# Kernel optimization log

Hardware: AMD Instinct MI355X
Metric: run time of the kernel (lower is better)

## Reference

```python
import jax, jax.numpy as jnp
import numpy as np

N_ITERS = 3  # Set2Set n_iters


def _set2set(feat, gid, B, Wih, Whh, bih, bhh):
    # DGL Set2Set with n_iters=3, n_layers=1: LSTM(input=2D, hidden=D), PyTorch gate order i,f,g,o
    N, D = feat.shape
    q_star = jnp.zeros((B, 2 * D), feat.dtype)
    h = jnp.zeros((B, D), feat.dtype)
    c = jnp.zeros((B, D), feat.dtype)
    bias = bih + bhh
    for _ in range(N_ITERS):
        gates = q_star @ Wih.T + h @ Whh.T + bias  # (B, 4D)
        i, f, g, o = jnp.split(gates, 4, axis=-1)
        i = jax.nn.sigmoid(i); f = jax.nn.sigmoid(f); o = jax.nn.sigmoid(o); g = jnp.tanh(g)
        c = f * c + i * g
        h = o * jnp.tanh(c)  # q = h, shape (B, D)
        e = jnp.sum(feat * h[gid], axis=-1)  # (N,) attention logits
        m = jax.ops.segment_max(e, gid, num_segments=B, indices_are_sorted=True)
        ex = jnp.exp(e - m[gid])
        s = jax.ops.segment_sum(ex, gid, num_segments=B, indices_are_sorted=True)
        alpha = ex / s[gid]  # segment softmax
        readout = jax.ops.segment_sum(feat * alpha[:, None], gid, num_segments=B, indices_are_sorted=True)
        q_star = jnp.concatenate([h, readout], axis=-1)  # (B, 2D)
    return q_star


def setup_inputs() -> dict:
    key = jax.random.key(0)
    ks = jax.random.split(key, 18)
    N, E, D, B, OUT = 100000, 1000000, 64, 64, 1
    s = 1.0 / np.sqrt(D)
    u = lambda k, shp, b: jax.random.uniform(k, shp, jnp.float32, -b, b)
    inp = {
        'feat': jax.random.normal(ks[0], (N, D), jnp.float32),
        'efeat': jax.random.normal(ks[1], (E, D), jnp.float32),
        'edge_dst': jax.random.randint(ks[2], (E,), 0, N, jnp.int32),
        'node_graph': jnp.sort(jax.random.randint(ks[3], (N,), 0, B, jnp.int32)),
        'n_graphs': B,
        'node_Wih': u(ks[4], (4 * D, 2 * D), s), 'node_Whh': u(ks[5], (4 * D, D), s),
        'node_bih': u(ks[6], (4 * D,), s), 'node_bhh': u(ks[7], (4 * D,), s),
        'edge_Wih': u(ks[8], (4 * D, 2 * D), s), 'edge_Whh': u(ks[9], (4 * D, D), s),
        'edge_bih': u(ks[10], (4 * D,), s), 'edge_bhh': u(ks[11], (4 * D,), s),
        'W1': u(ks[12], (32, 4 * D), np.sqrt(6.0 / (4 * D + 32)) * np.sqrt(2.0)),
        'b1': jnp.zeros((32,), jnp.float32),
        'W2': u(ks[13], (16, 32), np.sqrt(6.0 / 48) * np.sqrt(2.0)),
        'b2': jnp.zeros((16,), jnp.float32),
        'W3': u(ks[14], (OUT, 16), np.sqrt(6.0 / (16 + OUT)) * np.sqrt(2.0)),
        'b3': jnp.zeros((OUT,), jnp.float32),
    }
    return inp


def reference(feat, efeat, edge_dst, node_graph, n_graphs,
              node_Wih, node_Whh, node_bih, node_bhh,
              edge_Wih, edge_Whh, edge_bih, edge_bhh,
              W1, b1, W2, b2, W3, b3):
    N = feat.shape[0]
    # mpnn = identity: node_emb = feat, edge_emb = efeat
    node_s2s = _set2set(feat, node_graph, n_graphs, node_Wih, node_Whh, node_bih, node_bhh)
    # graph.update_all(fn.copy_e, fn.mean): scatter-mean of edge features onto dst nodes
    deg = jax.ops.segment_sum(jnp.ones((efeat.shape[0],), feat.dtype), edge_dst, num_segments=N)
    edge_agg = jax.ops.segment_sum(efeat, edge_dst, num_segments=N) / jnp.maximum(deg, 1.0)[:, None]
    edge_s2s = _set2set(edge_agg, node_graph, n_graphs, edge_Wih, edge_Whh, edge_bih, edge_bhh)
    out = jnp.concatenate([node_s2s, edge_s2s], axis=1)  # (B, 4D)
    out = jax.nn.relu(out @ W1.T + b1)
    out = jax.nn.relu(out @ W2.T + b2)
    out = out @ W3.T + b3
    return out
```

## Files before the change

kernel.cpp:

```cpp
#include <hip/hip_runtime.h>
#include <math.h>

#define D 64
#define B 64
#define NPB 256
#define NSLOT 4
#define SCAN_BS 1024

__device__ __forceinline__ unsigned encf(float x) {
  unsigned u = __float_as_uint(x);
  return (u & 0x80000000u) ? ~u : (u | 0x80000000u);
}
__device__ __forceinline__ float decf(unsigned e) {
  return (e & 0x80000000u) ? __uint_as_float(e ^ 0x80000000u) : __uint_as_float(~e);
}
__device__ __forceinline__ float sigm(float x) { return 1.0f / (1.0f + expf(-x)); }


__global__ void k_deg(const int* __restrict__ edge_dst, int* __restrict__ deg, int E) {
  int i = blockIdx.x * blockDim.x + threadIdx.x;
  if (i < E) atomicAdd(&deg[edge_dst[i]], 1);
}

__global__ void k_scan1(const int* __restrict__ deg, int* __restrict__ row_start,
                        int* __restrict__ blocksum, int N) {
  __shared__ int sm[SCAN_BS];
  int t = threadIdx.x;
  int base = blockIdx.x * SCAN_BS;
  int v = (base + t < N) ? deg[base + t] : 0;
  sm[t] = v;
  __syncthreads();
  for (int ofs = 1; ofs < SCAN_BS; ofs <<= 1) {
    int add = (t >= ofs) ? sm[t - ofs] : 0;
    __syncthreads();
    sm[t] += add;
    __syncthreads();
  }
  if (base + t < N) row_start[base + t] = sm[t] - v;
  if (t == SCAN_BS - 1) blocksum[blockIdx.x] = sm[t];
}

__global__ void k_scan2(int* __restrict__ blocksum, int nb) {
  __shared__ int sm[128];
  int t = threadIdx.x;
  int v = (t < nb) ? blocksum[t] : 0;
  sm[t] = v;
  __syncthreads();
  for (int ofs = 1; ofs < 128; ofs <<= 1) {
    int add = (t >= ofs) ? sm[t - ofs] : 0;
    __syncthreads();
    sm[t] += add;
    __syncthreads();
  }
  if (t < nb) blocksum[t] = sm[t] - v;
}

__global__ void k_scan3(int* __restrict__ row_start, const int* __restrict__ blocksum,
                        int* __restrict__ cursor, int N) {
  int n = blockIdx.x * blockDim.x + threadIdx.x;
  if (n < N) {
    int v = row_start[n] + blocksum[n / SCAN_BS];
    row_start[n] = v;
    cursor[n] = v;
  }
}

__global__ void k_fill(const int* __restrict__ edge_dst, int* __restrict__ cursor,
                       int* __restrict__ csr, int E) {
  int e = blockIdx.x * blockDim.x + threadIdx.x;
  if (e < E) {
    int dst = edge_dst[e];
    int idx = atomicAdd(&cursor[dst], 1);
    csr[idx] = e;
  }
}


struct AttSmem {
  float r_lds[16 * NSLOT * D];
  float s_lds[16 * NSLOT];
  float m_lds[16 * NSLOT];
  float h_lds[NSLOT * D];
  float o_lds[NSLOT];
  int used[NSLOT];
  int sg_first;
};

__device__ __forceinline__ void att_body(AttSmem* sm, const float* __restrict__ F,
                                         const int* __restrict__ gid,
                                         const float* __restrict__ h,
                                         const float* __restrict__ off,
                                         unsigned* __restrict__ m_enc,
                                         float* __restrict__ s_buf,
                                         float* __restrict__ r_buf,
                                         int N, int bx) {
  const int tid = threadIdx.x;
  const int grp = tid >> 4;
  const int d4  = tid & 15;
  const int base = bx * NPB;

  for (int i = tid; i < 16 * NSLOT * D; i += 256) sm->r_lds[i] = 0.0f;
  if (tid < 16 * NSLOT) { sm->s_lds[tid] = 0.0f; sm->m_lds[tid] = -3.4e38f; }
  if (tid < NSLOT) sm->used[tid] = 0;
  if (tid == 0) sm->sg_first = gid[base];
  __syncthreads();
  const int gfirst = sm->sg_first;
  {
    int slot = tid >> 6, dim = tid & 63;
    int g = gfirst + slot;
    if (g < B) {
      sm->h_lds[tid] = h[g * D + dim];
      if (dim == 0) sm->o_lds[slot] = off[g];
    }
  }
  __syncthreads();

  float4 acc = make_float4(0.f, 0.f, 0.f, 0.f);
  float sum_ex = 0.0f;
  float local_max = -3.4e38f;
  int cur_g = -1;

  for (int itn = 0; itn < NPB / 32; ++itn) {
    int n0 = base + itn * 32 + grp;
    int n1 = n0 + 16;
    bool ok0 = n0 < N, ok1 = n1 < N;
    int g0 = ok0 ? gid[n0] : -1;
    int g1 = ok1 ? gid[n1] : -1;
    float4 f0 = make_float4(0,0,0,0), f1 = make_float4(0,0,0,0);
    float dot0 = 0.f, dot1 = 0.f, ex0 = 0.f, ex1 = 0.f;
    if (ok0) {
      f0 = *(const float4*)(F + (size_t)n0 * D + d4 * 4);
      int s0 = g0 - gfirst;
      float4 hv = (s0 >= 0 && s0 < NSLOT) ? *(const float4*)&sm->h_lds[(s0 << 6) + (d4 << 2)]
                                          : *(const float4*)(h + (size_t)g0 * D + d4 * 4);
      dot0 = f0.x * hv.x + f0.y * hv.y + f0.z * hv.z + f0.w * hv.w;
    }
    if (ok1) {
      f1 = *(const float4*)(F + (size_t)n1 * D + d4 * 4);
      int s1 = g1 - gfirst;
      float4 hv = (s1 >= 0 && s1 < NSLOT) ? *(const float4*)&sm->h_lds[(s1 << 6) + (d4 << 2)]
                                          : *(const float4*)(h + (size_t)g1 * D + d4 * 4);
      dot1 = f1.x * hv.x + f1.y * hv.y + f1.z * hv.z + f1.w * hv.w;
    }
    dot0 += __shfl_xor(dot0, 1); dot1 += __shfl_xor(dot1, 1);
    dot0 += __shfl_xor(dot0, 2); dot1 += __shfl_xor(dot1, 2);
    dot0 += __shfl_xor(dot0, 4); dot1 += __shfl_xor(dot1, 4);
    dot0 += __shfl_xor(dot0, 8); dot1 += __shfl_xor(dot1, 8);
    if (ok0) {
      int s0 = g0 - gfirst;
      ex0 = expf(dot0 - ((s0 >= 0 && s0 < NSLOT) ? sm->o_lds[s0] : off[g0]));
    }
    if (ok1) {
      int s1 = g1 - gfirst;
      ex1 = expf(dot1 - ((s1 >= 0 && s1 < NSLOT) ? sm->o_lds[s1] : off[g1]));
    }

    #pragma unroll
    for (int pair = 0; pair < 2; ++pair) {
      bool ok = pair ? ok1 : ok0;
      int g = pair ? g1 : g0;
      float ex = pair ? ex1 : ex0;
      float dt = pair ? dot1 : dot0;
      float4 f = pair ? f1 : f0;
      if (!ok) continue;
      if (g != cur_g) {
        if (cur_g >= 0) {
          int slot = cur_g - gfirst;
          if (slot >= 0 && slot < NSLOT) {
            float4* p = (float4*)&sm->r_lds[((grp * NSLOT + slot) << 6) + (d4 << 2)];
            float4 v = *p;
            v.x += acc.x; v.y += acc.y; v.z += acc.z; v.w += acc.w;
            *p = v;
            if (d4 == 0) {
              sm->s_lds[grp * NSLOT + slot] += sum_ex;
              sm->m_lds[grp * NSLOT + slot] = fmaxf(sm->m_lds[grp * NSLOT + slot], local_max);
              sm->used[slot] = 1;
            }
          } else {
            float* rp = r_buf + cur_g * D + d4 * 4;
            atomicAdd(rp + 0, acc.x); atomicAdd(rp + 1, acc.y);
            atomicAdd(rp + 2, acc.z); atomicAdd(rp + 3, acc.w);
            if (d4 == 0) { atomicAdd(&s_buf[cur_g], sum_ex); atomicMax(&m_enc[cur_g], encf(local_max)); }
          }
        }
        cur_g = g; acc = make_float4(0,0,0,0); sum_ex = 0.f; local_max = -3.4e38f;
      }
      acc.x += ex * f.x; acc.y += ex * f.y; acc.z += ex * f.z; acc.w += ex * f.w;
      if (d4 == 0) { sum_ex += ex; local_max = fmaxf(local_max, dt); }
    }
  }
  if (cur_g >= 0) {
    int slot = cur_g - gfirst;
    if (slot >= 0 && slot < NSLOT) {
      float4* p = (float4*)&sm->r_lds[((grp * NSLOT + slot) << 6) + (d4 << 2)];
      float4 v = *p;
      v.x += acc.x; v.y += acc.y; v.z += acc.z; v.w += acc.w;
      *p = v;
      if (d4 == 0) {
        sm->s_lds[grp * NSLOT + slot] += sum_ex;
        sm->m_lds[grp * NSLOT + slot] = fmaxf(sm->m_lds[grp * NSLOT + slot], local_max);
        sm->used[slot] = 1;
      }
    } else {
      float* rp = r_buf + cur_g * D + d4 * 4;
      atomicAdd(rp + 0, acc.x); atomicAdd(rp + 1, acc.y);
      atomicAdd(rp + 2, acc.z); atomicAdd(rp + 3, acc.w);
      if (d4 == 0) { atomicAdd(&s_buf[cur_g], sum_ex); atomicMax(&m_enc[cur_g], encf(local_max)); }
    }
  }
  __syncthreads();

  {
    int slot = tid >> 6, dim = tid & 63;
    int g = gfirst + slot;
    if (g < B && sm->used[slot]) {
      float sum = 0.0f;
      #pragma unroll
      for (int q = 0; q < 16; ++q) sum += sm->r_lds[((q * NSLOT + slot) << 6) + dim];
      atomicAdd(&r_buf[g * D + dim], sum);
    }
  }
  if (tid < NSLOT) {
    int g = gfirst + tid;
    if (g < B && sm->used[tid]) {
      float ssum = 0.0f;
      #pragma unroll
      for (int q = 0; q < 16; ++q) ssum += sm->s_lds[q * NSLOT + tid];
      atomicAdd(&s_buf[g], ssum);
    }
  } else if (tid >= 64 && tid < 64 + NSLOT) {
    int slot = tid - 64;
    int g = gfirst + slot;
    if (g < B && sm->used[slot]) {
      float mmax = -3.4e38f;
      #pragma unroll
      for (int q = 0; q < 16; ++q) mmax = fmaxf(mmax, sm->m_lds[q * NSLOT + slot]);
      atomicMax(&m_enc[g], encf(mmax));
    }
  }
}

__device__ __forceinline__ void gather_body(const float* __restrict__ efeat,
                                            const int* __restrict__ csr,
                                            const int* __restrict__ row_start,
                                            const int* __restrict__ deg,
                                            float* __restrict__ edge_agg, int N, int bx) {
  int grp = (bx * 256 + threadIdx.x) >> 4;
  int l16 = threadIdx.x & 15;
  if (grp >= N) return;
  int base = row_start[grp];
  int dg = deg[grp];
  float4 acc = make_float4(0.f, 0.f, 0.f, 0.f);
  for (int i = 0; i < dg; i += 16) {
    int idx[16];
    #pragma unroll
    for (int j = 0; j < 16; ++j) {
      int k = i + j;
      idx[j] = csr[base + (k < dg ? k : dg - 1)];
    }
    #pragma unroll
    for (int j = 0; j < 16; ++j) {
      float4 v = *(const float4*)(efeat + (size_t)idx[j] * D + l16 * 4);
      bool ok = (i + j < dg);
      acc.x += ok ? v.x : 0.0f;
      acc.y += ok ? v.y : 0.0f;
      acc.z += ok ? v.z : 0.0f;
      acc.w += ok ? v.w : 0.0f;
    }
  }
  float inv = 1.0f / fmaxf((float)dg, 1.0f);
  acc.x *= inv; acc.y *= inv; acc.z *= inv; acc.w *= inv;
  *(float4*)(edge_agg + (size_t)grp * D + l16 * 4) = acc;
}

__global__ void k_gather_att0(int GB, const float* __restrict__ efeat,
                              const int* __restrict__ csr, const int* __restrict__ row_start,
                              const int* __restrict__ deg, float* __restrict__ edge_agg,
                              const float* __restrict__ feat, const int* __restrict__ gid,
                              const float* __restrict__ h2, const float* __restrict__ off2,
                              unsigned* __restrict__ m2, float* __restrict__ s2,
                              float* __restrict__ r2, int N) {
  __shared__ AttSmem sm;
  if ((int)blockIdx.x < GB) {
    gather_body(efeat, csr, row_start, deg, edge_agg, N, blockIdx.x);
  } else {
    att_body(&sm, feat, gid, h2, off2, m2, s2, r2, N, blockIdx.x - GB);
  }
}

__global__ void k_att(int side_base, const float* __restrict__ feat,
                      const float* __restrict__ edge_agg, const int* __restrict__ gid,
                      const float* __restrict__ h2, const float* __restrict__ off2,
                      unsigned* __restrict__ m2, float* __restrict__ s2,
                      float* __restrict__ r2, int N) {
  __shared__ AttSmem sm;
  int side = blockIdx.y + side_base;
  att_body(&sm, side ? edge_agg : feat, gid, h2 + side * B * D, off2 + side * B,
           m2 + side * B, s2 + side * B, r2 + side * B * D, N, blockIdx.x);
}


__global__ void k_lstm(int firstN, int firstE, int side_base,
                       float* __restrict__ h2, float* __restrict__ c2,
                       float* __restrict__ s2, float* __restrict__ r2,
                       unsigned* __restrict__ m2, float* __restrict__ off2,
                       const float* __restrict__ nWih, const float* __restrict__ nWhh,
                       const float* __restrict__ nbih, const float* __restrict__ nbhh,
                       const float* __restrict__ eWih, const float* __restrict__ eWhh,
                       const float* __restrict__ ebih, const float* __restrict__ ebhh) {
  __shared__ float lq[2 * D], lsg[4 * D];
  int side = blockIdx.y + side_base;
  int first = side ? firstE : firstN;
  const float* Wih = side ? eWih : nWih;
  const float* Whh = side ? eWhh : nWhh;
  const float* bih = side ? ebih : nbih;
  const float* bhh = side ? ebhh : nbhh;
  float* h = h2 + side * B * D;
  float* c = c2 + side * B * D;
  float* s_buf = s2 + side * B;
  float* r_buf = r2 + side * B * D;
  unsigned* m_enc = m2 + side * B;
  float* off = off2 + side * B;

  int b = blockIdx.x, j = threadIdx.x;
  if (j < D) {
    lq[j] = h[b * D + j];
  } else if (j < 2 * D) {
    lq[j] = first ? 0.0f : (r_buf[b * D + (j - D)] / s_buf[b]);
  }
  __syncthreads();
  float acc = bih[j] + bhh[j];
  const float* wr = Wih + (size_t)j * (2 * D);
  #pragma unroll 8
  for (int k = 0; k < 2 * D; ++k) acc += lq[k] * wr[k];
  const float* wr2 = Whh + (size_t)j * D;
  #pragma unroll 8
  for (int k = 0; k < D; ++k) acc += lq[k] * wr2[k];
  lsg[j] = acc;
  __syncthreads();
  if (j < D) {
    float ig = sigm(lsg[j]);
    float fg = sigm(lsg[D + j]);
    float gg = tanhf(lsg[2 * D + j]);
    float og = sigm(lsg[3 * D + j]);
    float cn = fg * c[b * D + j] + ig * gg;
    c[b * D + j] = cn;
    h[b * D + j] = og * tanhf(cn);
    r_buf[b * D + j] = 0.0f;
  }
  if (j == D) s_buf[b] = 0.0f;
  if (j == D + 1) {
    off[b] = first ? 0.0f : decf(m_enc[b]);
    m_enc[b] = 0u;
  }
}


__global__ void k_mlp(const float* __restrict__ h2, const float* __restrict__ r2,
                      const float* __restrict__ s2,
                      const float* __restrict__ W1, const float* __restrict__ b1,
                      const float* __restrict__ W2, const float* __restrict__ b2,
                      const float* __restrict__ W3, const float* __restrict__ b3,
                      float* __restrict__ out) {
  __shared__ float x[4 * D], h1[32], h2s[16];
  int b = blockIdx.x, t = threadIdx.x;
  x[t]       = (t < D) ? h2[b * D + t]         : r2[b * D + (t - D)] / s2[b];
  x[128 + t] = (t < D) ? h2[B * D + b * D + t] : r2[B * D + b * D + (t - D)] / s2[B + b];
  __syncthreads();
  if (t < 32) {
    float acc = b1[t];
    const float* w = W1 + (size_t)t * (4 * D);
    #pragma unroll 8
    for (int k = 0; k < 4 * D; ++k) acc += x[k] * w[k];
    h1[t] = fmaxf(acc, 0.0f);
  }
  __syncthreads();
  if (t < 16) {
    float acc = b2[t];
    const float* w = W2 + (size_t)t * 32;
    #pragma unroll
    for (int k = 0; k < 32; ++k) acc += h1[k] * w[k];
    h2s[t] = fmaxf(acc, 0.0f);
  }
  __syncthreads();
  if (t == 0) {
    float acc = b3[0];
    #pragma unroll
    for (int k = 0; k < 16; ++k) acc += h2s[k] * W3[k];
    out[b] = acc;
  }
}


extern "C" void kernel_launch(void* const* d_in, const int* in_sizes, int n_in,
                              void* d_out, int out_size, void* d_ws, size_t ws_size,
                              hipStream_t stream) {
  const float* feat      = (const float*)d_in[0];
  const float* efeat     = (const float*)d_in[1];
  const int*   edge_dst  = (const int*)d_in[2];
  const int*   node_graph= (const int*)d_in[3];
  const float* node_Wih  = (const float*)d_in[5];
  const float* node_Whh  = (const float*)d_in[6];
  const float* node_bih  = (const float*)d_in[7];
  const float* node_bhh  = (const float*)d_in[8];
  const float* edge_Wih  = (const float*)d_in[9];
  const float* edge_Whh  = (const float*)d_in[10];
  const float* edge_bih  = (const float*)d_in[11];
  const float* edge_bhh  = (const float*)d_in[12];
  const float* W1 = (const float*)d_in[13];
  const float* b1 = (const float*)d_in[14];
  const float* W2 = (const float*)d_in[15];
  const float* b2 = (const float*)d_in[16];
  const float* W3 = (const float*)d_in[17];
  const float* b3 = (const float*)d_in[18];
  float* out = (float*)d_out;

  const int N = in_sizes[0] / D;
  const int E = in_sizes[2];

  float* ws = (float*)d_ws;
  size_t off = 0;
  float* edge_agg = ws + off; off += (size_t)N * D;
  float* h2       = ws + off; off += 2 * B * D;
  float* c2       = ws + off; off += 2 * B * D;
  float* s2       = ws + off; off += 2 * B;
  float* r2       = ws + off; off += 2 * B * D;
  float* off2     = ws + off; off += 2 * B;
  unsigned* m2    = (unsigned*)(ws + off); off += 2 * B;
  int* deg        = (int*)(ws + off); off += N;
  int* row_start  = (int*)(ws + off); off += N;
  int* cursor     = (int*)(ws + off); off += N;
  int* blocksum   = (int*)(ws + off); off += 128;
  int* csr        = (int*)(ws + off); off += E + 8;

  hipMemsetAsync(deg, 0, (size_t)N * sizeof(int), stream);
  hipMemsetAsync(h2, 0, (size_t)(4 * B * D) * sizeof(float), stream);

  const int nb = (N + SCAN_BS - 1) / SCAN_BS;
  k_deg<<<(E + 255) / 256, 256, 0, stream>>>(edge_dst, deg, E);
  k_scan1<<<nb, SCAN_BS, 0, stream>>>(deg, row_start, blocksum, N);
  k_scan2<<<1, 128, 0, stream>>>(blocksum, nb);
  k_scan3<<<(N + 255) / 256, 256, 0, stream>>>(row_start, blocksum, cursor, N);
  k_fill<<<(E + 255) / 256, 256, 0, stream>>>(edge_dst, cursor, csr, E);

  const int att_blocks = (N + NPB - 1) / NPB;
  const int GB = (N + 15) / 16;

  k_lstm<<<dim3(B, 1), 256, 0, stream>>>(1, 0, 0, h2, c2, s2, r2, m2, off2,
      node_Wih, node_Whh, node_bih, node_bhh, edge_Wih, edge_Whh, edge_bih, edge_bhh);
  k_gather_att0<<<GB + att_blocks, 256, 0, stream>>>(GB, efeat, csr, row_start, deg, edge_agg,
      feat, node_graph, h2, off2, m2, s2, r2, N);
  k_lstm<<<dim3(B, 2), 256, 0, stream>>>(0, 1, 0, h2, c2, s2, r2, m2, off2,
      node_Wih, node_Whh, node_bih, node_bhh, edge_Wih, edge_Whh, edge_bih, edge_bhh);
  k_att<<<dim3(att_blocks, 2), 256, 0, stream>>>(0, feat, edge_agg, node_graph, h2, off2, m2, s2, r2, N);
  k_lstm<<<dim3(B, 2), 256, 0, stream>>>(0, 0, 0, h2, c2, s2, r2, m2, off2,
      node_Wih, node_Whh, node_bih, node_bhh, edge_Wih, edge_Whh, edge_bih, edge_bhh);
  k_att<<<dim3(att_blocks, 2), 256, 0, stream>>>(0, feat, edge_agg, node_graph, h2, off2, m2, s2, r2, N);
  k_lstm<<<dim3(B, 1), 256, 0, stream>>>(0, 0, 1, h2, c2, s2, r2, m2, off2,
      node_Wih, node_Whh, node_bih, node_bhh, edge_Wih, edge_Whh, edge_bih, edge_bhh);
  k_att<<<dim3(att_blocks, 1), 256, 0, stream>>>(1, feat, edge_agg, node_graph, h2, off2, m2, s2, r2, N);

  k_mlp<<<B, 128, 0, stream>>>(h2, r2, s2, W1, b1, W2, b2, W3, b3, out);
}
```

Baseline: 285.2 us.

## Overlap CSR fill and edge gather with node-side attention iterations

The schedule is reorganized so the CSR fill kernel runs alongside the first node-side attention pass and the edge gather runs alongside the second node-side pass. Only the third node iteration then pairs with the first edge iteration, and the edge side finishes with two single-side passes. The change also halves nodes per attention block to spread work over more blocks and switches exp to the fast __expf intrinsic. In exchange there are more kernel launches on the edge tail, slightly lower exp precision, and possible underutilisation in the single-side tail passes.

```diff
diff --git a/kernel.cpp b/kernel.cpp
--- a/kernel.cpp
+++ b/kernel.cpp
@@ -3,7 +3,7 @@
 
 #define D 64
 #define B 64
-#define NPB 256
+#define NPB 128
 #define NSLOT 4
 #define SCAN_BS 1024
 
@@ -14,7 +14,7 @@
 __device__ __forceinline__ float decf(unsigned e) {
   return (e & 0x80000000u) ? __uint_as_float(e ^ 0x80000000u) : __uint_as_float(~e);
 }
-__device__ __forceinline__ float sigm(float x) { return 1.0f / (1.0f + expf(-x)); }
+__device__ __forceinline__ float sigm(float x) { return 1.0f / (1.0f + __expf(-x)); }
 
 
 __global__ void k_deg(const int* __restrict__ edge_dst, int* __restrict__ deg, int E) {
@@ -62,16 +62,6 @@
     int v = row_start[n] + blocksum[n / SCAN_BS];
     row_start[n] = v;
     cursor[n] = v;
-  }
-}
-
-__global__ void k_fill(const int* __restrict__ edge_dst, int* __restrict__ cursor,
-                       int* __restrict__ csr, int E) {
-  int e = blockIdx.x * blockDim.x + threadIdx.x;
-  if (e < E) {
-    int dst = edge_dst[e];
-    int idx = atomicAdd(&cursor[dst], 1);
-    csr[idx] = e;
   }
 }
 
@@ -148,11 +138,11 @@
     dot0 += __shfl_xor(dot0, 8); dot1 += __shfl_xor(dot1, 8);
     if (ok0) {
       int s0 = g0 - gfirst;
-      ex0 = expf(dot0 - ((s0 >= 0 && s0 < NSLOT) ? sm->o_lds[s0] : off[g0]));
+      ex0 = __expf(dot0 - ((s0 >= 0 && s0 < NSLOT) ? sm->o_lds[s0] : off[g0]));
     }
     if (ok1) {
       int s1 = g1 - gfirst;
-      ex1 = expf(dot1 - ((s1 >= 0 && s1 < NSLOT) ? sm->o_lds[s1] : off[g1]));
+      ex1 = __expf(dot1 - ((s1 >= 0 && s1 < NSLOT) ? sm->o_lds[s1] : off[g1]));
     }
 
     #pragma unroll
@@ -273,18 +263,39 @@
   *(float4*)(edge_agg + (size_t)grp * D + l16 * 4) = acc;
 }
 
-__global__ void k_gather_att0(int GB, const float* __restrict__ efeat,
-                              const int* __restrict__ csr, const int* __restrict__ row_start,
-                              const int* __restrict__ deg, float* __restrict__ edge_agg,
-                              const float* __restrict__ feat, const int* __restrict__ gid,
-                              const float* __restrict__ h2, const float* __restrict__ off2,
-                              unsigned* __restrict__ m2, float* __restrict__ s2,
-                              float* __restrict__ r2, int N) {
+__global__ void k_att_fill(int ATT, const float* __restrict__ feat, const int* __restrict__ gid,
+                           const float* __restrict__ h2, const float* __restrict__ off2,
+                           unsigned* __restrict__ m2, float* __restrict__ s2,
+                           float* __restrict__ r2, int N,
+                           const int* __restrict__ edge_dst, int* __restrict__ cursor,
+                           int* __restrict__ csr, int E) {
   __shared__ AttSmem sm;
-  if ((int)blockIdx.x < GB) {
-    gather_body(efeat, csr, row_start, deg, edge_agg, N, blockIdx.x);
+  int bx = blockIdx.x;
+  if (bx < ATT) {
+    att_body(&sm, feat, gid, h2, off2, m2, s2, r2, N, bx);
   } else {
-    att_body(&sm, feat, gid, h2, off2, m2, s2, r2, N, blockIdx.x - GB);
+    int e = (bx - ATT) * 256 + threadIdx.x;
+    if (e < E) {
+      int dst = edge_dst[e];
+      int idx = atomicAdd(&cursor[dst], 1);
+      csr[idx] = e;
+    }
+  }
+}
+
+__global__ void k_att_gather(int ATT, const float* __restrict__ feat, const int* __restrict__ gid,
+                             const float* __restrict__ h2, const float* __restrict__ off2,
+                             unsigned* __restrict__ m2, float* __restrict__ s2,
+                             float* __restrict__ r2, int N,
+                             const float* __restrict__ efeat, const int* __restrict__ csr,
+                             const int* __restrict__ row_start, const int* __restrict__ deg,
+                             float* __restrict__ edge_agg) {
+  __shared__ AttSmem sm;
+  int bx = blockIdx.x;
+  if (bx < ATT) {
+    att_body(&sm, feat, gid, h2, off2, m2, s2, r2, N, bx);
+  } else {
+    gather_body(efeat, csr, row_start, deg, edge_agg, N, bx - ATT);
   }
 }
 
@@ -308,7 +319,7 @@
                        const float* __restrict__ nbih, const float* __restrict__ nbhh,
                        const float* __restrict__ eWih, const float* __restrict__ eWhh,
                        const float* __restrict__ ebih, const float* __restrict__ ebhh) {
-  __shared__ float lq[2 * D], lsg[4 * D];
+  __shared__ float sq[2 * D], sg[4 * D];
   int side = blockIdx.y + side_base;
   int first = side ? firstE : firstN;
   const float* Wih = side ? eWih : nWih;
@@ -319,30 +330,28 @@
   float* c = c2 + side * B * D;
   float* s_buf = s2 + side * B;
   float* r_buf = r2 + side * B * D;
-  unsigned* m_enc = m2 + side * B;
-  float* off = off2 + side * B;
 
   int b = blockIdx.x, j = threadIdx.x;
   if (j < D) {
-    lq[j] = h[b * D + j];
+    sq[j] = h[b * D + j];
   } else if (j < 2 * D) {
-    lq[j] = first ? 0.0f : (r_buf[b * D + (j - D)] / s_buf[b]);
+    sq[j] = first ? 0.0f : (r_buf[b * D + (j - D)] / s_buf[b]);
   }
   __syncthreads();
   float acc = bih[j] + bhh[j];
   const float* wr = Wih + (size_t)j * (2 * D);
   #pragma unroll 8
-  for (int k = 0; k < 2 * D; ++k) acc += lq[k] * wr[k];
+  for (int k = 0; k < 2 * D; ++k) acc += sq[k] * wr[k];
   const float* wr2 = Whh + (size_t)j * D;
   #pragma unroll 8
-  for (int k = 0; k < D; ++k) acc += lq[k] * wr2[k];
-  lsg[j] = acc;
+  for (int k = 0; k < D; ++k) acc += sq[k] * wr2[k];
+  sg[j] = acc;
   __syncthreads();
   if (j < D) {
-    float ig = sigm(lsg[j]);
-    float fg = sigm(lsg[D + j]);
-    float gg = tanhf(lsg[2 * D + j]);
-    float og = sigm(lsg[3 * D + j]);
+    float ig = sigm(sg[j]);
+    float fg = sigm(sg[D + j]);
+    float gg = tanhf(sg[2 * D + j]);
+    float og = sigm(sg[3 * D + j]);
     float cn = fg * c[b * D + j] + ig * gg;
     c[b * D + j] = cn;
     h[b * D + j] = og * tanhf(cn);
@@ -350,8 +359,9 @@
   }
   if (j == D) s_buf[b] = 0.0f;
   if (j == D + 1) {
-    off[b] = first ? 0.0f : decf(m_enc[b]);
-    m_enc[b] = 0u;
+    int idx = side * B + b;
+    off2[idx] = first ? 0.0f : decf(m2[idx]);
+    m2[idx] = 0u;
   }
 }
 
@@ -437,28 +447,32 @@
   hipMemsetAsync(h2, 0, (size_t)(4 * B * D) * sizeof(float), stream);
 
   const int nb = (N + SCAN_BS - 1) / SCAN_BS;
+  const int ATT = (N + NPB - 1) / NPB;
+  const int FB = (E + 255) / 256;
+  const int GB = (N + 15) / 16;
+
   k_deg<<<(E + 255) / 256, 256, 0, stream>>>(edge_dst, deg, E);
   k_scan1<<<nb, SCAN_BS, 0, stream>>>(deg, row_start, blocksum, N);
   k_scan2<<<1, 128, 0, stream>>>(blocksum, nb);
   k_scan3<<<(N + 255) / 256, 256, 0, stream>>>(row_start, blocksum, cursor, N);
-  k_fill<<<(E + 255) / 256, 256, 0, stream>>>(edge_dst, cursor, csr, E);
-
-  const int att_blocks = (N + NPB - 1) / NPB;
-  const int GB = (N + 15) / 16;
 
   k_lstm<<<dim3(B, 1), 256, 0, stream>>>(1, 0, 0, h2, c2, s2, r2, m2, off2,
       node_Wih, node_Whh, node_bih, node_bhh, edge_Wih, edge_Whh, edge_bih, edge_bhh);
-  k_gather_att0<<<GB + att_blocks, 256, 0, stream>>>(GB, efeat, csr, row_start, deg, edge_agg,
-      feat, node_graph, h2, off2, m2, s2, r2, N);
+  k_att_fill<<<ATT + FB, 256, 0, stream>>>(ATT, feat, node_graph, h2, off2, m2, s2, r2, N,
+      edge_dst, cursor, csr, E);
+  k_lstm<<<dim3(B, 1), 256, 0, stream>>>(0, 0, 0, h2, c2, s2, r2, m2, off2,
+      node_Wih, node_Whh, node_bih, node_bhh, edge_Wih, edge_Whh, edge_bih, edge_bhh);
+  k_att_gather<<<ATT + GB, 256, 0, stream>>>(ATT, feat, node_graph, h2, off2, m2, s2, r2, N,
+      efeat, csr, row_start, deg, edge_agg);
   k_lstm<<<dim3(B, 2), 256, 0, stream>>>(0, 1, 0, h2, c2, s2, r2, m2, off2,
       node_Wih, node_Whh, node_bih, node_bhh, edge_Wih, edge_Whh, edge_bih, edge_bhh);
-  k_att<<<dim3(att_blocks, 2), 256, 0, stream>>>(0, feat, edge_agg, node_graph, h2, off2, m2, s2, r2, N);
-  k_lstm<<<dim3(B, 2), 256, 0, stream>>>(0, 0, 0, h2, c2, s2, r2, m2, off2,
-      node_Wih, node_Whh, node_bih, node_bhh, edge_Wih, edge_Whh, edge_bih, edge_bhh);
-  k_att<<<dim3(att_blocks, 2), 256, 0, stream>>>(0, feat, edge_agg, node_graph, h2, off2, m2, s2, r2, N);
+  k_att<<<dim3(ATT, 2), 256, 0, stream>>>(0, feat, edge_agg, node_graph, h2, off2, m2, s2, r2, N);
   k_lstm<<<dim3(B, 1), 256, 0, stream>>>(0, 0, 1, h2, c2, s2, r2, m2, off2,
       node_Wih, node_Whh, node_bih, node_bhh, edge_Wih, edge_Whh, edge_bih, edge_bhh);
-  k_att<<<dim3(att_blocks, 1), 256, 0, stream>>>(1, feat, edge_agg, node_graph, h2, off2, m2, s2, r2, N);
+  k_att<<<dim3(ATT, 1), 256, 0, stream>>>(1, feat, edge_agg, node_graph, h2, off2, m2, s2, r2, N);
+  k_lstm<<<dim3(B, 1), 256, 0, stream>>>(0, 0, 1, h2, c2, s2, r2, m2, off2,
+      node_Wih, node_Whh, node_bih, node_bhh, edge_Wih, edge_Whh, edge_bih, edge_bhh);
+  k_att<<<dim3(ATT, 1), 256, 0, stream>>>(1, feat, edge_agg, node_graph, h2, off2, m2, s2, r2, N);
 
   k_mlp<<<B, 128, 0, stream>>>(h2, r2, s2, W1, b1, W2, b2, W3, b3, out);
 }
```

Result: faster. 263.0 us (-7.8%).
